# Kernel tuning notes

Hardware: AMD Instinct MI355X
Metric: run time of the kernel (lower is better)

## Reference

```python
import jax, jax.numpy as jnp
import numpy as np

IN_DIM = 256
QK_DIM = IN_DIM // 8


def setup_inputs() -> dict:
    key = jax.random.key(0)
    ks = jax.random.split(key, 7)
    B, C, H, W = 4, IN_DIM, 64, 64
    s = 0.05
    return {
        "x": jax.random.normal(ks[0], (B, C, H, W), dtype=jnp.float32),
        "Wq": jax.random.normal(ks[1], (QK_DIM, C), dtype=jnp.float32) * s,
        "bq": jnp.zeros((QK_DIM,), dtype=jnp.float32),
        "Wk": jax.random.normal(ks[2], (QK_DIM, C), dtype=jnp.float32) * s,
        "bk": jnp.zeros((QK_DIM,), dtype=jnp.float32),
        "Wv": jax.random.normal(ks[3], (C, C), dtype=jnp.float32) * s,
        "bv": jnp.zeros((C,), dtype=jnp.float32),
        "gamma": jnp.zeros((1,), dtype=jnp.float32),
    }


def reference(x, Wq, bq, Wk, bk, Wv, bv, gamma):
    B, C, H, W = x.shape
    N = H * W
    xf = x.reshape(B, C, N)  # [B, C, N]
    # 1x1 convs are channel matmuls
    q = jnp.einsum('oc,bcn->bno', Wq, xf) + bq  # [B, N, Cqk]
    k = jnp.einsum('oc,bcn->bon', Wk, xf) + bk[None, :, None]  # [B, Cqk, N]
    energy = jnp.einsum('bno,bom->bnm', q, k)  # [B, N, N]
    attn = jax.nn.softmax(energy, axis=-1)
    v = jnp.einsum('oc,bcn->bon', Wv, xf) + bv[None, :, None]  # [B, C, N]
    # torch: out = bmm(v, attn^T) -> out[b,c,m] = sum_n v[b,c,n]*attn[m,n]
    out = jnp.einsum('bcn,bmn->bcm', v, attn)
    out = out.reshape(B, C, H, W)
    return gamma[0] * out + x
```

## Files before the change

kernel.cpp:

```cpp
#include <hip/hip_runtime.h>
#include <hip/hip_bf16.h>
#include <cstddef>

#define NB  4
#define NC  256
#define NN  4096
#define DQK 32
#define MT  64
#define JT  128
#define NIT (NN / JT)
#define XS2 264

typedef __attribute__((ext_vector_type(8))) short short8;
typedef __attribute__((ext_vector_type(4))) float f32x4;

#define MFMA16(a, b, c) __builtin_amdgcn_mfma_f32_16x16x32_bf16((a), (b), (c), 0, 0, 0)

__device__ inline unsigned pk2bf(float a, float b) {
  __hip_bfloat162 h = __float22bfloat162_rn(make_float2(a, b));
  unsigned u;
  __builtin_memcpy(&u, &h, 4);
  return u;
}

__device__ inline void bar_lgkm() {
  asm volatile("s_waitcnt lgkmcnt(0)" ::: "memory");
  __builtin_amdgcn_s_barrier();
  asm volatile("" ::: "memory");
}

__global__ __launch_bounds__(256) void wcvt_kernel(
    const float* __restrict__ Wq, const float* __restrict__ Wk,
    const float* __restrict__ Wv, __hip_bfloat16* __restrict__ W16) {
  const int id4 = (blockIdx.x * 256 + threadIdx.x) * 4;
  const int row = id4 >> 8, col = id4 & 255;
  const float* src = (row < 32) ? Wq + row * 256
                   : (row < 64) ? Wk + (row - 32) * 256
                                : Wv + (row - 64) * 256;
  float4 vv = *(const float4*)(src + col);
  *(uint2*)(W16 + id4) = make_uint2(pk2bf(vv.x, vv.y), pk2bf(vv.z, vv.w));
}

__global__ __launch_bounds__(256) void proj_kernel(
    const float* __restrict__ x, const __hip_bfloat16* __restrict__ W16,
    const float* __restrict__ bq, const float* __restrict__ bk,
    const float* __restrict__ bv, __hip_bfloat16* __restrict__ q,
    __hip_bfloat16* __restrict__ kT, __hip_bfloat16* __restrict__ v) {
  __shared__ __hip_bfloat16 Xs[32 * XS2];
  const int t = threadIdx.x;
  const int b = blockIdx.y, n0 = blockIdx.x * 32;
  const int w = __builtin_amdgcn_readfirstlane(t >> 6);
  const int ln = t & 15, quad = (t & 63) >> 4;
  const int sn = t & 31, scg = t >> 5;

  const float* xsrc = x + (size_t)b * NC * NN + n0 + sn;
  float xr[4][8];
#pragma unroll
  for (int g = 0; g < 4; ++g)
#pragma unroll
    for (int i = 0; i < 8; ++i)
      xr[g][i] = xsrc[(size_t)(g * 64 + scg * 8 + i) * NN];
#pragma unroll
  for (int g = 0; g < 4; ++g) {
    uint4 pw;
    pw.x = pk2bf(xr[g][0], xr[g][1]);
    pw.y = pk2bf(xr[g][2], xr[g][3]);
    pw.z = pk2bf(xr[g][4], xr[g][5]);
    pw.w = pk2bf(xr[g][6], xr[g][7]);
    *(uint4*)&Xs[sn * XS2 + g * 64 + scg * 8] = pw;
  }
  bar_lgkm();

  f32x4 zero4 = {0.f, 0.f, 0.f, 0.f};
  f32x4 acc[5][2];
#pragma unroll
  for (int i = 0; i < 5; ++i)
#pragma unroll
    for (int j = 0; j < 2; ++j) acc[i][j] = zero4;

#pragma unroll
  for (int k0 = 0; k0 < NC; k0 += 32) {
    short8 af[5], bfr[2];
#pragma unroll
    for (int ot = 0; ot < 5; ++ot)
      af[ot] = *(const short8*)(W16 + (size_t)(w * 80 + ot * 16 + ln) * NC + k0 + quad * 8);
#pragma unroll
    for (int nt = 0; nt < 2; ++nt)
      bfr[nt] = *(const short8*)&Xs[(nt * 16 + ln) * XS2 + k0 + quad * 8];
#pragma unroll
    for (int ot = 0; ot < 5; ++ot)
#pragma unroll
      for (int nt = 0; nt < 2; ++nt)
        acc[ot][nt] = MFMA16(af[ot], bfr[nt], acc[ot][nt]);
  }

#pragma unroll
  for (int ot = 0; ot < 5; ++ot) {
    const int gbase = w * 80 + ot * 16;
    if (gbase < 32) {
#pragma unroll
      for (int nt = 0; nt < 2; ++nt)
#pragma unroll
        for (int r = 0; r < 4; ++r) {
          const int row = gbase + quad * 4 + r;
          q[((size_t)b * NN + n0 + nt * 16 + ln) * DQK + row] =
              __hip_bfloat16(acc[ot][nt][r] + bq[row]);
        }
    } else if (gbase < 64) {
#pragma unroll
      for (int nt = 0; nt < 2; ++nt)
#pragma unroll
        for (int r = 0; r < 4; ++r) {
          const int row = gbase - 32 + quad * 4 + r;
          kT[((size_t)b * NN + n0 + nt * 16 + ln) * DQK + row] =
              __hip_bfloat16(acc[ot][nt][r] + bk[row]);
        }
    } else {
#pragma unroll
      for (int nt = 0; nt < 2; ++nt)
#pragma unroll
        for (int r = 0; r < 4; ++r) {
          const int c = gbase - 64 + quad * 4 + r;
          v[((size_t)b * NC + c) * NN + n0 + nt * 16 + ln] =
              __hip_bfloat16(acc[ot][nt][r] + bv[c]);
        }
    }
  }
}

__global__ __launch_bounds__(512, 2) void flash_kernel(
    const __hip_bfloat16* __restrict__ q, const __hip_bfloat16* __restrict__ kt,
    const __hip_bfloat16* __restrict__ v, const float* __restrict__ x,
    const float* __restrict__ gamma, float* __restrict__ out) {
  __shared__ __align__(16) __hip_bfloat16 Ps[2][MT * JT];
  __shared__ float lrow[MT];

  const int t  = threadIdx.x;
  const int bi = blockIdx.x;
  const int b  = (bi & 7) >> 1;
  const int m0 = (((bi & 1) * 32) + (bi >> 3)) * MT;

  const int w    = __builtin_amdgcn_readfirstlane(t >> 6);
  const int ln   = t & 15;
  const int quad = (t & 63) >> 4;

  const __hip_bfloat16* kb_base = kt + (size_t)b * NN * DQK;
  const __hip_bfloat16* v_base  = v + (size_t)b * NC * NN;

  if (w < 4) {
    const short8 qa =
        *(const short8*)(q + ((size_t)b * NN + m0 + w * 16 + ln) * DQK + quad * 8);
    float lreg = 0.f;
    const f32x4 zero4 = {0.f, 0.f, 0.f, 0.f};
    short8 kb[8];
#pragma unroll
    for (int jt = 0; jt < 8; ++jt)
      kb[jt] = *(const short8*)(kb_base + (size_t)(jt * 16 + ln) * DQK + quad * 8);

    const int m = w * 16 + ln;

    for (int it = 0; it < NIT; ++it) {
      f32x4 st[8];
      __builtin_amdgcn_s_setprio(1);
#pragma unroll
      for (int jt = 0; jt < 8; ++jt) st[jt] = MFMA16(kb[jt], qa, zero4);
      __builtin_amdgcn_s_setprio(0);

      if (it + 1 < NIT) {
        const int jn = (it + 1) * JT;
#pragma unroll
        for (int jt = 0; jt < 8; ++jt)
          kb[jt] = *(const short8*)(kb_base + (size_t)(jn + jt * 16 + ln) * DQK + quad * 8);
      }

      char* pbase = (char*)&Ps[it & 1][0] + m * (JT * 2);
#pragma unroll
      for (int jt = 0; jt < 8; ++jt) {
        const float e0 = __expf(st[jt][0]), e1 = __expf(st[jt][1]);
        const float e2 = __expf(st[jt][2]), e3 = __expf(st[jt][3]);
        lreg += (e0 + e1) + (e2 + e3);
        *(uint2*)(pbase + ((jt * 32 + quad * 8) ^ ((m & 7) << 4))) =
            make_uint2(pk2bf(e0, e1), pk2bf(e2, e3));
      }
      bar_lgkm();
    }
    lreg += __shfl_xor(lreg, 16);
    lreg += __shfl_xor(lreg, 32);
    if (quad == 0) lrow[w * 16 + ln] = lreg;
    bar_lgkm();
  } else {
    const int c0 = (w - 4) * 64;
    const f32x4 zero4 = {0.f, 0.f, 0.f, 0.f};
    f32x4 acc[4][4];
#pragma unroll
    for (int ct = 0; ct < 4; ++ct)
#pragma unroll
      for (int mt = 0; mt < 4; ++mt) acc[ct][mt] = zero4;

    short8 va[4][4];
#pragma unroll
    for (int ct = 0; ct < 4; ++ct)
#pragma unroll
      for (int ks = 0; ks < 4; ++ks)
        va[ct][ks] = *(const short8*)(v_base +
            (size_t)(c0 + ct * 16 + ln) * NN + ks * 32 + quad * 8);
    bar_lgkm();

    for (int it = 1; it < NIT; ++it) {
      const char* pbase = (const char*)&Ps[(it - 1) & 1][0];
      const int j0 = it * JT;
#pragma unroll
      for (int ks = 0; ks < 4; ++ks) {
        short8 pb[4];
#pragma unroll
        for (int mt = 0; mt < 4; ++mt)
          pb[mt] = *(const short8*)(pbase + (mt * 16 + ln) * (JT * 2) +
                                    ((ks * 64 + quad * 16) ^ ((ln & 7) << 4)));
        __builtin_amdgcn_s_setprio(1);
#pragma unroll
        for (int ct = 0; ct < 4; ++ct)
#pragma unroll
          for (int mt = 0; mt < 4; ++mt)
            acc[ct][mt] = MFMA16(va[ct][ks], pb[mt], acc[ct][mt]);
        __builtin_amdgcn_s_setprio(0);
#pragma unroll
        for (int ct = 0; ct < 4; ++ct)
          va[ct][ks] = *(const short8*)(v_base +
              (size_t)(c0 + ct * 16 + ln) * NN + j0 + ks * 32 + quad * 8);
      }
      bar_lgkm();
    }

    {
      const char* pbase = (const char*)&Ps[(NIT - 1) & 1][0];
#pragma unroll
      for (int ks = 0; ks < 4; ++ks) {
        short8 pb[4];
#pragma unroll
        for (int mt = 0; mt < 4; ++mt)
          pb[mt] = *(const short8*)(pbase + (mt * 16 + ln) * (JT * 2) +
                                    ((ks * 64 + quad * 16) ^ ((ln & 7) << 4)));
        __builtin_amdgcn_s_setprio(1);
#pragma unroll
        for (int ct = 0; ct < 4; ++ct)
#pragma unroll
          for (int mt = 0; mt < 4; ++mt)
            acc[ct][mt] = MFMA16(va[ct][ks], pb[mt], acc[ct][mt]);
        __builtin_amdgcn_s_setprio(0);
      }
    }
    bar_lgkm();

    const float g0 = gamma[0];
    float li[4];
#pragma unroll
    for (int mt = 0; mt < 4; ++mt) li[mt] = 1.f / lrow[mt * 16 + ln];
#pragma unroll
    for (int ct = 0; ct < 4; ++ct)
#pragma unroll
      for (int r = 0; r < 4; ++r) {
        const int c = c0 + ct * 16 + quad * 4 + r;
        const float* xr = x + ((size_t)b * NC + c) * NN + m0;
        float* orow = out + ((size_t)b * NC + c) * NN + m0;
#pragma unroll
        for (int mt = 0; mt < 4; ++mt) {
          const int m = mt * 16 + ln;
          orow[m] = g0 * (acc[ct][mt][r] * li[mt]) + xr[m];
        }
      }
  }
}

extern "C" void kernel_launch(void* const* d_in, const int* in_sizes, int n_in,
                              void* d_out, int out_size, void* d_ws, size_t ws_size,
                              hipStream_t stream) {
  const float* x     = (const float*)d_in[0];
  const float* Wq    = (const float*)d_in[1];
  const float* bq    = (const float*)d_in[2];
  const float* Wk    = (const float*)d_in[3];
  const float* bk    = (const float*)d_in[4];
  const float* Wv    = (const float*)d_in[5];
  const float* bv    = (const float*)d_in[6];
  const float* gamma = (const float*)d_in[7];
  float* out = (float*)d_out;

  char* wsp = (char*)d_ws;
  __hip_bfloat16* W16 = (__hip_bfloat16*)wsp;  wsp += (size_t)320 * NC * 2;
  __hip_bfloat16* q   = (__hip_bfloat16*)wsp;  wsp += (size_t)NB * NN * DQK * 2;
  __hip_bfloat16* kT  = (__hip_bfloat16*)wsp;  wsp += (size_t)NB * NN * DQK * 2;
  __hip_bfloat16* v   = (__hip_bfloat16*)wsp;

  wcvt_kernel<<<dim3(80), dim3(256), 0, stream>>>(Wq, Wk, Wv, W16);
  proj_kernel<<<dim3(NN / 32, NB), dim3(256), 0, stream>>>(x, W16, bq, bk, bv, q, kT, v);
  flash_kernel<<<dim3(NB * NN / MT), dim3(512), 0, stream>>>(q, kT, v, x, gamma, out);
}
```

Baseline: 171.7 us.

## Stage K and V tiles into LDS via direct global-to-LDS loads

Halves the key tile width and stages both K and V tiles through double-buffered LDS using global_load_lds, with XOR-swizzled layouts. Previously the PV waves kept V in registers and the QK waves kept K in registers, both loaded straight from global memory. Every wave now issues the async copies, and the custom lgkm barrier is replaced by __syncthreads. The larger LDS footprint (Vs is 64KB) may limit occupancy below the two blocks per CU the launch bounds request, and the smaller tile doubles the number of barriers.

Result: faster. 167.1 us (-2.6%).

```diff
diff --git a/kernel.cpp b/kernel.cpp
--- a/kernel.cpp
+++ b/kernel.cpp
@@ -7,7 +7,7 @@
 #define NN  4096
 #define DQK 32
 #define MT  64
-#define JT  128
+#define JT  64
 #define NIT (NN / JT)
 #define XS2 264
 
@@ -23,10 +23,10 @@
   return u;
 }
 
-__device__ inline void bar_lgkm() {
-  asm volatile("s_waitcnt lgkmcnt(0)" ::: "memory");
-  __builtin_amdgcn_s_barrier();
-  asm volatile("" ::: "memory");
+__device__ inline void gl16(const void* g, void* s) {
+  __builtin_amdgcn_global_load_lds(
+      (const __attribute__((address_space(1))) void*)g,
+      (__attribute__((address_space(3))) void*)s, 16, 0, 0);
 }
 
 __global__ __launch_bounds__(256) void wcvt_kernel(
@@ -69,7 +69,7 @@
     pw.w = pk2bf(xr[g][6], xr[g][7]);
     *(uint4*)&Xs[sn * XS2 + g * 64 + scg * 8] = pw;
   }
-  bar_lgkm();
+  __syncthreads();
 
   f32x4 zero4 = {0.f, 0.f, 0.f, 0.f};
   f32x4 acc[5][2];
@@ -132,6 +132,8 @@
     const __hip_bfloat16* __restrict__ q, const __hip_bfloat16* __restrict__ kt,
     const __hip_bfloat16* __restrict__ v, const float* __restrict__ x,
     const float* __restrict__ gamma, float* __restrict__ out) {
+  __shared__ __align__(16) __hip_bfloat16 Ks[2][JT * DQK];
+  __shared__ __align__(16) __hip_bfloat16 Vs[2][NC * JT];
   __shared__ __align__(16) __hip_bfloat16 Ps[2][MT * JT];
   __shared__ float lrow[MT];
 
@@ -141,53 +143,66 @@
   const int m0 = (((bi & 1) * 32) + (bi >> 3)) * MT;
 
   const int w    = __builtin_amdgcn_readfirstlane(t >> 6);
+  const int l    = t & 63;
   const int ln   = t & 15;
   const int quad = (t & 63) >> 4;
 
   const __hip_bfloat16* kb_base = kt + (size_t)b * NN * DQK;
   const __hip_bfloat16* v_base  = v + (size_t)b * NC * NN;
+
+  size_t voff[4];
+#pragma unroll
+  for (int k = 0; k < 4; ++k) {
+    const int g = w * 4 + k;
+    const int c = g * 8 + (l >> 3);
+    voff[k] = (size_t)c * NN + (((l & 7) ^ ((l >> 3) & 7)) * 8);
+  }
+  const size_t koff = (size_t)(w * 16 + (l >> 2)) * DQK +
+                      (((l & 3) ^ ((l >> 2) & 3)) * 8);
+
+  if (w < 4) gl16(kb_base + koff, &Ks[0][w * 512]);
+  __syncthreads();
 
   if (w < 4) {
     const short8 qa =
         *(const short8*)(q + ((size_t)b * NN + m0 + w * 16 + ln) * DQK + quad * 8);
     float lreg = 0.f;
     const f32x4 zero4 = {0.f, 0.f, 0.f, 0.f};
-    short8 kb[8];
-#pragma unroll
-    for (int jt = 0; jt < 8; ++jt)
-      kb[jt] = *(const short8*)(kb_base + (size_t)(jt * 16 + ln) * DQK + quad * 8);
-
     const int m = w * 16 + ln;
 
     for (int it = 0; it < NIT; ++it) {
-      f32x4 st[8];
+#pragma unroll
+      for (int k = 0; k < 4; ++k)
+        gl16(v_base + voff[k] + (size_t)it * JT, &Vs[it & 1][(w * 4 + k) * 512]);
+      if (it + 1 < NIT)
+        gl16(kb_base + koff + (size_t)(it + 1) * JT * DQK, &Ks[(it + 1) & 1][w * 512]);
+
+      short8 kb[4];
+#pragma unroll
+      for (int jt = 0; jt < 4; ++jt)
+        kb[jt] = *(const short8*)&Ks[it & 1][(jt * 16 + ln) * DQK +
+                                            ((quad ^ (ln & 3)) * 8)];
+      f32x4 st[4];
       __builtin_amdgcn_s_setprio(1);
 #pragma unroll
-      for (int jt = 0; jt < 8; ++jt) st[jt] = MFMA16(kb[jt], qa, zero4);
+      for (int jt = 0; jt < 4; ++jt) st[jt] = MFMA16(kb[jt], qa, zero4);
       __builtin_amdgcn_s_setprio(0);
 
-      if (it + 1 < NIT) {
-        const int jn = (it + 1) * JT;
-#pragma unroll
-        for (int jt = 0; jt < 8; ++jt)
-          kb[jt] = *(const short8*)(kb_base + (size_t)(jn + jt * 16 + ln) * DQK + quad * 8);
-      }
-
       char* pbase = (char*)&Ps[it & 1][0] + m * (JT * 2);
 #pragma unroll
-      for (int jt = 0; jt < 8; ++jt) {
+      for (int jt = 0; jt < 4; ++jt) {
         const float e0 = __expf(st[jt][0]), e1 = __expf(st[jt][1]);
         const float e2 = __expf(st[jt][2]), e3 = __expf(st[jt][3]);
         lreg += (e0 + e1) + (e2 + e3);
         *(uint2*)(pbase + ((jt * 32 + quad * 8) ^ ((m & 7) << 4))) =
             make_uint2(pk2bf(e0, e1), pk2bf(e2, e3));
       }
-      bar_lgkm();
+      __syncthreads();
     }
     lreg += __shfl_xor(lreg, 16);
     lreg += __shfl_xor(lreg, 32);
     if (quad == 0) lrow[w * 16 + ln] = lreg;
-    bar_lgkm();
+    __syncthreads();
   } else {
     const int c0 = (w - 4) * 64;
     const f32x4 zero4 = {0.f, 0.f, 0.f, 0.f};
@@ -197,44 +212,52 @@
 #pragma unroll
       for (int mt = 0; mt < 4; ++mt) acc[ct][mt] = zero4;
 
-    short8 va[4][4];
-#pragma unroll
-    for (int ct = 0; ct < 4; ++ct)
-#pragma unroll
-      for (int ks = 0; ks < 4; ++ks)
-        va[ct][ks] = *(const short8*)(v_base +
-            (size_t)(c0 + ct * 16 + ln) * NN + ks * 32 + quad * 8);
-    bar_lgkm();
-
-    for (int it = 1; it < NIT; ++it) {
-      const char* pbase = (const char*)&Ps[(it - 1) & 1][0];
-      const int j0 = it * JT;
-#pragma unroll
-      for (int ks = 0; ks < 4; ++ks) {
-        short8 pb[4];
-#pragma unroll
-        for (int mt = 0; mt < 4; ++mt)
-          pb[mt] = *(const short8*)(pbase + (mt * 16 + ln) * (JT * 2) +
-                                    ((ks * 64 + quad * 16) ^ ((ln & 7) << 4)));
-        __builtin_amdgcn_s_setprio(1);
+    for (int it = 0; it < NIT; ++it) {
+#pragma unroll
+      for (int k = 0; k < 4; ++k)
+        gl16(v_base + voff[k] + (size_t)it * JT, &Vs[it & 1][(w * 4 + k) * 512]);
+
+      if (it > 0) {
+        const int pbuf = (it - 1) & 1;
+        const char* pbase = (const char*)&Ps[pbuf][0];
+        short8 va[4][2];
 #pragma unroll
         for (int ct = 0; ct < 4; ++ct)
 #pragma unroll
+          for (int ks = 0; ks < 2; ++ks)
+            va[ct][ks] = *(const short8*)&Vs[pbuf][
+                (c0 + ct * 16 + ln) * JT + (((ks * 4 + quad) ^ (ln & 7)) * 8)];
+#pragma unroll
+        for (int ks = 0; ks < 2; ++ks) {
+          short8 pb[4];
+#pragma unroll
           for (int mt = 0; mt < 4; ++mt)
-            acc[ct][mt] = MFMA16(va[ct][ks], pb[mt], acc[ct][mt]);
-        __builtin_amdgcn_s_setprio(0);
-#pragma unroll
-        for (int ct = 0; ct < 4; ++ct)
-          va[ct][ks] = *(const short8*)(v_base +
-              (size_t)(c0 + ct * 16 + ln) * NN + j0 + ks * 32 + quad * 8);
+            pb[mt] = *(const short8*)(pbase + (mt * 16 + ln) * (JT * 2) +
+                                      ((ks * 64 + quad * 16) ^ ((ln & 7) << 4)));
+          __builtin_amdgcn_s_setprio(1);
+#pragma unroll
+          for (int ct = 0; ct < 4; ++ct)
+#pragma unroll
+            for (int mt = 0; mt < 4; ++mt)
+              acc[ct][mt] = MFMA16(va[ct][ks], pb[mt], acc[ct][mt]);
+          __builtin_amdgcn_s_setprio(0);
+        }
       }
-      bar_lgkm();
+      __syncthreads();
     }
 
     {
-      const char* pbase = (const char*)&Ps[(NIT - 1) & 1][0];
-#pragma unroll
-      for (int ks = 0; ks < 4; ++ks) {
+      const int pbuf = (NIT - 1) & 1;
+      const char* pbase = (const char*)&Ps[pbuf][0];
+      short8 va[4][2];
+#pragma unroll
+      for (int ct = 0; ct < 4; ++ct)
+#pragma unroll
+        for (int ks = 0; ks < 2; ++ks)
+          va[ct][ks] = *(const short8*)&Vs[pbuf][
+              (c0 + ct * 16 + ln) * JT + (((ks * 4 + quad) ^ (ln & 7)) * 8)];
+#pragma unroll
+      for (int ks = 0; ks < 2; ++ks) {
         short8 pb[4];
 #pragma unroll
         for (int mt = 0; mt < 4; ++mt)
@@ -249,7 +272,7 @@
         __builtin_amdgcn_s_setprio(0);
       }
     }
-    bar_lgkm();
+    __syncthreads();
 
     const float g0 = gamma[0];
     float li[4];
```
